# Optimization experiments

Hardware: AMD Instinct MI355X
Metric: run time of the kernel (lower is better)

## Reference

```python
import jax, jax.numpy as jnp
import numpy as np

EPS = 1e-5

def _dh_grid(b):
    # Driscoll-Healy beta grid + quadrature weights (includes sin(beta))
    k = np.arange(2 * b)
    beta = np.pi * (2 * k + 1) / (4 * b)
    j = np.arange(b)
    w = (2.0 / b) * np.sin(beta) * (np.sin(np.outer(beta, 2 * j + 1)) / (2 * j + 1)).sum(1)
    return beta, w

def _wigner_stack(L, betas):
    # d^l_{m m'}(beta) for l<L, zero-padded to slots j=m+(L-1) in a [L,nb,2L-1,2L-1] array.
    betas = np.atleast_1d(np.asarray(betas, np.float64))
    nb = betas.shape[0]
    J = 2 * L - 1
    out = np.zeros((L, nb, J, J), np.float64)
    for l in range(L):
        if l == 0:
            d = np.ones((nb, 1, 1))
        else:
            m = np.arange(-l, l + 1)
            c = np.sqrt(l * (l + 1) - m[:-1] * (m[:-1] + 1.0))
            Jp = np.diag(c, -1).astype(complex)  # raising operator in m=-l..l basis
            Jy = (Jp - Jp.T) / 2j
            ev, V = np.linalg.eigh(Jy)
            ph = np.exp(-1j * betas[:, None] * ev[None, :])
            d = np.einsum('mk,bk,nk->bmn', V, ph, V.conj()).real
        s = (L - 1) - l
        out[l, :, s:s + 2 * l + 1, s:s + 2 * l + 1] = d
    return out

def _constants():
    C = {}
    # layer1: S2 conv b 64 -> 20
    beta1, wq1 = _dh_grid(64)
    d1 = _wigner_stack(20, beta1)
    C['s2_ana'] = jnp.asarray((d1[:, :, :, 19] * wq1[None, :, None] * (2 * np.pi / 128)).astype(np.float32))  # [20,128,39]
    C['half1'] = jnp.asarray(_wigner_stack(20, np.pi / 2)[:, 0, :, 19].astype(np.float32))  # [20,39]
    beta_o1, wq2 = _dh_grid(20)
    ls1 = (2 * np.arange(20) + 1.0)
    C['syn1'] = jnp.asarray((_wigner_stack(20, beta_o1) * ls1[:, None, None, None]).astype(np.float32))  # [20,40,39,39]
    # layer2: SO3 conv b 20 -> 10
    d2 = _wigner_stack(10, beta_o1)
    C['ana2'] = jnp.asarray((d2 * wq2[None, :, None, None] * (2 * np.pi / 40) ** 2).astype(np.float32))  # [10,40,19,19]
    C['half2'] = jnp.asarray(_wigner_stack(10, np.pi / 2)[:, 0].astype(np.float32))  # [10,19,19]
    beta_o2, wq3 = _dh_grid(10)
    ls2 = (2 * np.arange(10) + 1.0)
    C['syn2'] = jnp.asarray((_wigner_stack(10, beta_o2) * ls2[:, None, None, None]).astype(np.float32))  # [10,20,19,19]
    # layer3: SO3 conv b 10 -> 7
    C['ana3'] = jnp.asarray((_wigner_stack(7, beta_o2) * wq3[None, :, None, None] * (2 * np.pi / 20) ** 2).astype(np.float32))  # [7,20,13,13]
    C['half3'] = jnp.asarray(_wigner_stack(7, np.pi / 2)[:, 0].astype(np.float32))  # [7,13,13]
    beta_o3, _ = _dh_grid(7)
    ls3 = (2 * np.arange(7) + 1.0)
    C['syn3'] = jnp.asarray((_wigner_stack(7, beta_o3) * ls3[:, None, None, None]).astype(np.float32))  # [7,14,13,13]
    return C

_C = _constants()

def _so3_ifft(Z, L, d_syn):
    # Z: [L, J, J, B, O] spectral (zero padded); output [B, O, 2L(beta), 2L(alpha), 2L(gamma)]
    M = jnp.einsum('lkjn,ljnbo->bokjn', d_syn, Z)
    N = 2 * L
    J = 2 * L - 1
    idx = (np.arange(J) - (L - 1)) % N
    S = jnp.zeros(M.shape[:3] + (N, N), M.dtype).at[..., idx[:, None], idx[None, :]].set(M)
    return jnp.fft.fft2(S, axes=(-2, -1)).real

def _s2_conv(x, w, bias, C):
    # x: [B, F, 2b_in(beta), 2b_in(alpha)] -> [B, O, 2*20, 2*20, 2*20]
    B, F, K, N = x.shape
    L = 20
    J = 2 * L - 1
    m = np.arange(J) - (L - 1)
    xh = jnp.fft.fft(x, axis=-1)[..., m % N]                       # [B,F,K,J]
    Fx = jnp.einsum('lkj,bfkj->ljbf', C['s2_ana'], xh)             # spherical FFT
    P = w.shape[-1]
    alpha = 2 * np.pi * np.arange(P) / P
    e = jnp.asarray(np.exp(-1j * np.outer(m, alpha)).astype(np.complex64))
    scale = 1.0 / np.sqrt(P * F)
    Ky = jnp.einsum('lj,jp,fop->ljfo', C['half1'], e, w * scale)   # kernel RFT on equatorial grid
    Z = jnp.einsum('ljbf,lnfo->ljnbo', Fx, jnp.conj(Ky))           # s2_mm (outer product over m,n)
    return _so3_ifft(Z, L, C['syn1']) + bias[None, :, None, None, None]

def _so3_conv(x, w, bias, Lo, ana, half, syn):
    # x: [B, F, K(beta), N(alpha), N(gamma)] -> [B, O, 2Lo, 2Lo, 2Lo]
    B, F, K, N, _ = x.shape
    J = 2 * Lo - 1
    m = np.arange(J) - (Lo - 1)
    idx = (-m) % N
    xh = jnp.fft.fft2(x, axes=(-2, -1))[..., idx[:, None], idx[None, :]]  # [B,F,K,J,J]
    Fx = jnp.einsum('lkjn,bfkjn->ljnbf', ana, xh)                  # SO3 FFT
    P = w.shape[-1]
    alpha = 2 * np.pi * np.arange(P) / P
    e = jnp.asarray(np.exp(1j * np.outer(m, alpha)).astype(np.complex64))
    scale = 1.0 / np.sqrt(P * F)
    Ky = jnp.einsum('ljn,jp,fop->ljnfo', half, e, w * scale)       # kernel RFT (beta=pi/2, gamma=0 grid)
    Z = jnp.einsum('ljkbf,lnkfo->ljnbo', Fx, jnp.conj(Ky))         # so3_mm: Z_{mn}=sum_k Fx_{mk} conj(Ky_{nk})
    return _so3_ifft(Z, Lo, syn) + bias[None, :, None, None, None]

def _bn(x, gamma, beta):
    axes = (0,) + tuple(range(2, x.ndim))
    mu = x.mean(axes, keepdims=True)
    var = x.var(axes, keepdims=True)
    shp = (1, -1) + (1,) * (x.ndim - 2)
    return (x - mu) * jax.lax.rsqrt(var + EPS) * gamma.reshape(shp) + beta.reshape(shp)

def _forward(x, w1, b1, g1, bt1, w2, b2, g2, bt2, w3, b3, g3, bt3, w_out, b_out):
    x = _s2_conv(x, w1, b1, _C)
    x = jax.nn.relu(_bn(x, g1, bt1))
    x = _so3_conv(x, w2, b2, 10, _C['ana2'], _C['half2'], _C['syn2'])
    x = jax.nn.relu(_bn(x, g2, bt2))
    x = _so3_conv(x, w3, b3, 7, _C['ana3'], _C['half3'], _C['syn3'])
    x = jax.nn.relu(_bn(x, g3, bt3))
    x = x.reshape(x.shape[0], x.shape[1], -1).max(-1)              # global max pool over SO3 grid
    mu = x.mean(0, keepdims=True)
    var = x.var(0, keepdims=True)
    x = (x - mu) * jax.lax.rsqrt(var + EPS)                        # BatchNorm1d(affine=False)
    x = x @ w_out + b_out
    return jax.nn.log_softmax(x, axis=1)

def setup_inputs():
    key = jax.random.key(0)
    ks = jax.random.split(key, 6)
    B = 16
    return {
        'x': jax.random.normal(ks[0], (B, 6, 128, 128), jnp.float32),
        'w1': jax.random.normal(ks[1], (6, 20, 128), jnp.float32),
        'b1': jnp.zeros((20,), jnp.float32),
        'g1': jnp.ones((20,), jnp.float32),
        'bt1': jnp.zeros((20,), jnp.float32),
        'w2': jax.random.normal(ks[2], (20, 60, 40), jnp.float32),
        'b2': jnp.zeros((60,), jnp.float32),
        'g2': jnp.ones((60,), jnp.float32),
        'bt2': jnp.zeros((60,), jnp.float32),
        'w3': jax.random.normal(ks[3], (60, 100, 20), jnp.float32),
        'b3': jnp.zeros((100,), jnp.float32),
        'g3': jnp.ones((100,), jnp.float32),
        'bt3': jnp.zeros((100,), jnp.float32),
        'w_out': jax.random.normal(ks[4], (100, 55), jnp.float32) * 0.1,
        'b_out': jnp.zeros((55,), jnp.float32),
    }

def reference(x, w1, b1, g1, bt1, w2, b2, g2, bt2, w3, b3, g3, bt3, w_out, b_out):
    return _forward(x, w1, b1, g1, bt1, w2, b2, g2, bt2, w3, b3, g3, bt3, w_out, b_out)
```

## Files before the change

kernel.cpp:

```cpp
#include <hip/hip_runtime.h>
#include <math.h>

#define PI 3.14159265358979323846

__device__ inline int iabs(int x){ return x < 0 ? -x : x; }

__device__ inline void cadd_mul(float2& acc, float2 a, float2 b){
    acc.x += a.x*b.x - a.y*b.y;
    acc.y += a.x*b.y + a.y*b.x;
}
__device__ inline void cadd_mulc(float2& acc, float2 a, float2 b){
    acc.x += a.x*b.x + a.y*b.y;
    acc.y += a.y*b.x - a.x*b.y;
}

__device__ inline double dpowi(double x, int n){
    double r = 1.0;
    for (int i = 0; i < n; ++i) r *= x;
    return r;
}

__device__ double wigner_d(int l, int a, int b, double beta, const double* sf)
{
    double cb = cos(0.5*beta), sb = sin(0.5*beta);
    int smin = max(0, b - a);
    int smax = min(l + b, l - a);
    if (smin > smax) return 0.0;
    double pref = sqrt(sf[l+a]*sf[l-a]*sf[l+b]*sf[l-b]);
    double t = dpowi(cb, 2*l + b - a - 2*smin) * dpowi(sb, a - b + 2*smin);
    if ((a - b + smin) & 1) t = -t;
    double r = -(sb*sb)/(cb*cb);
    double sum = 0.0;
    for (int s = smin; s <= smax; ++s){
        sum += t / (sf[l+b-s]*sf[s]*sf[a-b+s]*sf[l-a-s]);
        t *= r;
    }
    return pref * sum;
}

__global__ void k_wq(double* wq)
{
    int i = blockIdx.x*blockDim.x + threadIdx.x;
    int b, k, off;
    if (i < 128){ b = 64; k = i;      off = 0;   }
    else if (i < 168){ b = 20; k = i-128; off = 128; }
    else if (i < 188){ b = 10; k = i-168; off = 168; }
    else return;
    double beta = PI*(2*k+1)/(4.0*b);
    double s = 0.0;
    for (int j = 0; j < b; ++j) s += sin((2*j+1)*beta)/(2*j+1);
    wq[off+k] = (2.0/b)*sin(beta)*s;
}

__global__ void k_wig_full(float* __restrict__ out, const double* __restrict__ wq,
                           int L, int J, int NB, double denom, double beta_fix,
                           double factor, int mul2l1, int klayout)
{
    __shared__ double sf[40];
    if (threadIdx.x == 0){ sf[0]=1.0; for (int i=1;i<40;i++) sf[i]=sf[i-1]*i; }
    __syncthreads();
    int idx = blockIdx.x*blockDim.x + threadIdx.x;
    int total = L*NB*J*J;
    if (idx >= total) return;
    int n = idx % J;
    int j = (idx/J) % J;
    int k = (idx/(J*J)) % NB;
    int l = idx/(J*J*NB);
    int c0 = (J-1)/2;
    int mj = j - c0, mn = n - c0;
    float v = 0.f;
    if (iabs(mj) <= l && iabs(mn) <= l){
        double beta = (denom > 0.0) ? PI*(2*k+1)/denom : beta_fix;
        double d = wigner_d(l, mj, mn, beta, sf);
        double mlt = factor * (mul2l1 ? (2.0*l + 1.0) : 1.0);
        if (wq) mlt *= wq[k];
        v = (float)(d*mlt);
    }
    size_t oidx = klayout ? ((size_t)(k*L + l)*J + j)*J + n
                          : ((size_t)(l*NB + k)*J + j)*J + n;
    out[oidx] = v;
}

__global__ void k_wig_col(float* __restrict__ out, const double* __restrict__ wq,
                          int L, int J, int NB, double denom, double beta_fix, double factor)
{
    __shared__ double sf[40];
    if (threadIdx.x == 0){ sf[0]=1.0; for (int i=1;i<40;i++) sf[i]=sf[i-1]*i; }
    __syncthreads();
    int idx = blockIdx.x*blockDim.x + threadIdx.x;
    int total = L*NB*J;
    if (idx >= total) return;
    int j = idx % J;
    int k = (idx/J) % NB;
    int l = idx/(J*NB);
    int mj = j - (J-1)/2;
    float v = 0.f;
    if (iabs(mj) <= l){
        double beta = (denom > 0.0) ? PI*(2*k+1)/denom : beta_fix;
        double d = wigner_d(l, mj, 0, beta, sf);
        double mlt = factor;
        if (wq) mlt *= wq[k];
        v = (float)(d*mlt);
    }
    out[idx] = v;
}

__global__ void k_expmat(float2* __restrict__ out, int R, int C, int r0, int c0, int N, double sgn)
{
    int i = blockIdx.x*blockDim.x + threadIdx.x;
    if (i >= R*C) return;
    int c = i % C, r = i / C;
    double ang = sgn*2.0*PI * (double)((r - r0)*(c - c0)) / (double)N;
    out[i] = make_float2((float)cos(ang), (float)sin(ang));
}

__global__ __launch_bounds__(256) void k_dft1(const float* __restrict__ x,
    const float2* __restrict__ E1, float2* __restrict__ xh)
{
    __shared__ float2 sE[4992];
    __shared__ float rows[2048];
    int r0 = blockIdx.x * 16;
    int tid = threadIdx.x;
    for (int i = tid; i < 4992; i += 256) sE[i] = E1[i];
    for (int i = tid; i < 2048; i += 256) rows[i] = x[(size_t)r0*128 + i];
    __syncthreads();
    for (int i = tid; i < 320; i += 256){
        int jj = i % 20, kl = i / 20;
        int j = jj + 19;
        const float* row = &rows[kl*128];
        float2 acc = make_float2(0.f, 0.f);
        for (int a = 0; a < 128; ++a){
            float v = row[a];
            float2 e = sE[a*39 + j];
            acc.x += v*e.x; acc.y += v*e.y;
        }
        xh[(size_t)(r0 + kl)*39 + j] = acc;
    }
}

__global__ void k_fx1(const float* __restrict__ ana, const float2* __restrict__ xh,
                      float2* __restrict__ Fx)
{
    int i = blockIdx.x*blockDim.x + threadIdx.x;
    if (i >= 400) return;
    int hj = i % 20, l = i / 20;
    int j = hj + 19;
    int bf = blockIdx.y;
    const float*  ar = ana + (size_t)l*4992 + j;
    const float2* xr = xh + (size_t)bf*4992 + j;
    float2 acc = make_float2(0.f, 0.f);
    for (int k = 0; k < 128; ++k){
        float a = ar[k*39];
        float2 v = xr[k*39];
        acc.x += a*v.x; acc.y += a*v.y;
    }
    Fx[(size_t)(l*39 + j)*96 + bf] = acc;
}

__global__ void k_wh(float2* __restrict__ wh, const float* __restrict__ w,
                     int J, int P, int F, int O, double sgn)
{
    __shared__ float2 tw[128];
    int tid = threadIdx.x;
    if (tid < P){
        double a = sgn*2.0*PI*tid/P;
        tw[tid] = make_float2((float)cos(a), (float)sin(a));
    }
    __syncthreads();
    int idx = blockIdx.x*blockDim.x + tid;
    if (idx >= J*F*O) return;
    int o = idx % O;
    int f = (idx/O) % F;
    int j = idx/(O*F);
    int mj = j - (J-1)/2;
    int step = ((mj % P) + P) % P;
    const float* wr = w + (f*O+o)*P;
    float2 acc = make_float2(0.f, 0.f);
    int t = 0;
    for (int p = 0; p < P; ++p){
        float v = wr[p];
        acc.x += v*tw[t].x; acc.y += v*tw[t].y;
        t += step; if (t >= P) t -= P;
    }
    wh[idx] = acc;
}

__global__ void k_z1(const float2* __restrict__ Fx, const float2* __restrict__ wh,
                     const float* __restrict__ half1, float2* __restrict__ Z1c, int b0)
{
    int i = blockIdx.x*blockDim.x + threadIdx.x;
    if (i >= 15600) return;
    int bo = blockIdx.y;
    int n = i % 39;
    int lh = i / 39;
    int hj = lh % 20, l = lh / 20;
    int j = hj + 19;
    int b = b0 + bo/20, o = bo % 20;
    float h = half1[l*39 + n] * (1.f/sqrtf(128.f*6.f));
    const float2* fx = Fx + (size_t)(l*39 + j)*96 + b*6;
    const float2* wv = wh + (size_t)n*120 + o;
    float2 acc = make_float2(0.f, 0.f);
    for (int f = 0; f < 6; ++f) cadd_mulc(acc, fx[f], wv[(size_t)f*20]);
    Z1c[(size_t)bo*15600 + i] = make_float2(acc.x*h, acc.y*h);
}

template<int L, int J, int K, int N, int O, int BS>
__global__ __launch_bounds__(BS) void k_idft_t(const float2* __restrict__ Z,
    const float* __restrict__ syn, const float2* __restrict__ W,
    const float* __restrict__ bias, float* __restrict__ out)
{
    constexpr int JJ = J*J, NN = N*N, c0 = (J-1)/2;
    constexpr int JH = (J+1)/2;
    constexpr int LHJ = L*JH*J;
    __shared__ float2 sM[JH*J];
    __shared__ float2 sT[JH*N];
    __shared__ float2 sW[J*N];
    int bid = blockIdx.x;
    int k = bid % K;
    int bo = bid / K;
    int tid = threadIdx.x;

    for (int i = tid; i < J*N; i += BS) sW[i] = W[i];

    for (int i = tid; i < JH*J; i += BS){
        int n = i % J, hj = i / J;
        int lmin = max(hj, iabs(n-c0));
        float2 acc = make_float2(0.f, 0.f);
        const float2* zrow = Z + (size_t)bo*LHJ + i;
        const float*  srow = syn + (size_t)k*L*JJ + (size_t)c0*J + i;
        for (int l = lmin; l < L; ++l){
            float s = srow[(size_t)l*JJ];
            float2 z = zrow[(size_t)l*(JH*J)];
            acc.x += s*z.x; acc.y += s*z.y;
        }
        sM[i] = acc;
    }
    __syncthreads();

    constexpr int RT = (JH+1)/2, CT = N/2;
    for (int t = tid; t < RT*CT; t += BS){
        int tg = t % CT, tj = t / CT;
        int h0 = tj*2, g0 = tg*2;
        int h1 = (h0+1 < JH) ? h0+1 : h0;
        float2 a00 = make_float2(0.f,0.f), a01 = make_float2(0.f,0.f);
        float2 a10 = make_float2(0.f,0.f), a11 = make_float2(0.f,0.f);
        for (int n = 0; n < J; ++n){
            float2 w0 = sW[n*N+g0], w1 = sW[n*N+g0+1];
            float2 m0 = sM[h0*J+n], m1 = sM[h1*J+n];
            cadd_mul(a00, m0, w0); cadd_mul(a01, m0, w1);
            cadd_mul(a10, m1, w0); cadd_mul(a11, m1, w1);
        }
        sT[h0*N+g0] = a00; sT[h0*N+g0+1] = a01;
        if (h0+1 < JH){ sT[(h0+1)*N+g0] = a10; sT[(h0+1)*N+g0+1] = a11; }
    }
    __syncthreads();

    float bb = bias[bo % O];
    float* obase = out + (size_t)bid*NN;
    for (int t = tid; t < CT*CT; t += BS){
        int tg = t % CT, ta = t / CT;
        int a0 = ta*2, g0 = tg*2;
        float2 t00 = sT[g0], t01 = sT[g0+1];
        float r00 = t00.x, r01 = t01.x, r10 = t00.x, r11 = t01.x;
        for (int hj = 1; hj < JH; ++hj){
            float2 wa0 = sW[(c0+hj)*N+a0], wa1 = sW[(c0+hj)*N+a0+1];
            float2 t0 = sT[hj*N+g0], t1 = sT[hj*N+g0+1];
            r00 += 2.f*(t0.x*wa0.x - t0.y*wa0.y);
            r01 += 2.f*(t1.x*wa0.x - t1.y*wa0.y);
            r10 += 2.f*(t0.x*wa1.x - t0.y*wa1.y);
            r11 += 2.f*(t1.x*wa1.x - t1.y*wa1.y);
        }
        obase[(a0+0)*N+g0]   = r00 + bb;
        obase[(a0+0)*N+g0+1] = r01 + bb;
        obase[(a0+1)*N+g0]   = r10 + bb;
        obase[(a0+1)*N+g0+1] = r11 + bb;
    }
}

__global__ __launch_bounds__(256) void k_bn_stats(const float4* __restrict__ x, double* __restrict__ part,
                                                  int B, int C, int S4, int parts)
{
    int c = blockIdx.y, p = blockIdx.x;
    int chunk = (S4 + parts - 1)/parts;
    int s0 = p*chunk, s1e = min(S4, s0 + chunk);
    double a1 = 0.0, a2 = 0.0;
    for (int b = 0; b < B; ++b){
        const float4* base = x + ((size_t)b*C + c)*S4;
        for (int s = s0 + threadIdx.x; s < s1e; s += 256){
            float4 v = base[s];
            a1 += (double)v.x + (double)v.y + (double)v.z + (double)v.w;
            a2 += (double)v.x*v.x + (double)v.y*v.y + (double)v.z*v.z + (double)v.w*v.w;
        }
    }
    __shared__ double r1[256], r2[256];
    r1[threadIdx.x] = a1; r2[threadIdx.x] = a2;
    __syncthreads();
    for (int off = 128; off > 0; off >>= 1){
        if (threadIdx.x < off){ r1[threadIdx.x] += r1[threadIdx.x+off]; r2[threadIdx.x] += r2[threadIdx.x+off]; }
        __syncthreads();
    }
    if (threadIdx.x == 0){ int bid = p*C + c; part[2*bid] = r1[0]; part[2*bid+1] = r2[0]; }
}

__global__ void k_bn_fin(const double* __restrict__ part, const float* __restrict__ g,
                         const float* __restrict__ bt, float2* __restrict__ scsh,
                         int C, int parts, double cnt)
{
    int c = blockIdx.x*blockDim.x + threadIdx.x;
    if (c >= C) return;
    double s1 = 0.0, s2 = 0.0;
    for (int p = 0; p < parts; ++p){ s1 += part[2*(p*C+c)]; s2 += part[2*(p*C+c)+1]; }
    double mu = s1/cnt;
    double var = s2/cnt - mu*mu;
    float sc = (float)(1.0/sqrt(var + 1e-5)) * g[c];
    float sh = bt[c] - (float)mu*sc;
    scsh[c] = make_float2(sc, sh);
}

__global__ __launch_bounds__(256) void k_bn_apply(float4* __restrict__ x, const float2* __restrict__ scsh,
                                                  int C, int S4)
{
    int bc = blockIdx.y;
    float2 p = scsh[bc % C];
    size_t base = (size_t)bc * S4;
    for (int s = blockIdx.x*256 + threadIdx.x; s < S4; s += gridDim.x*256){
        float4 v = x[base + s];
        v.x = fmaxf(fmaf(v.x, p.x, p.y), 0.f);
        v.y = fmaxf(fmaf(v.y, p.x, p.y), 0.f);
        v.z = fmaxf(fmaf(v.z, p.x, p.y), 0.f);
        v.w = fmaxf(fmaf(v.w, p.x, p.y), 0.f);
        x[base + s] = v;
    }
}

template<int N, int J>
__global__ __launch_bounds__(256) void k_dft2_t(const float* __restrict__ x, float2* __restrict__ xh,
                                                const float2* __restrict__ EF)
{
    constexpr int JH = (J+1)/2, c0 = (J-1)/2;
    constexpr int NP = N+1;
    __shared__ float tile[N*NP];
    __shared__ float2 sT[N*J];
    __shared__ float2 sE[N*J];
    int bid = blockIdx.x;
    int tid = threadIdx.x;
    const float* src = x + (size_t)bid*N*N;
    for (int i = tid; i < N*N; i += 256){
        int a = i / N, g = i % N;
        tile[a*NP + g] = src[i];
    }
    for (int i = tid; i < N*J; i += 256) sE[i] = EF[i];
    __syncthreads();
    constexpr int AT = N/2, NT = (J+1)/2;
    for (int t = tid; t < AT*NT; t += 256){
        int tn = t % NT, ta = t / NT;
        int a0 = 2*ta, n0 = 2*tn;
        int n1 = (n0+1 < J) ? n0+1 : n0;
        float2 a00 = make_float2(0.f,0.f), a01 = make_float2(0.f,0.f);
        float2 a10 = make_float2(0.f,0.f), a11 = make_float2(0.f,0.f);
        const float* r0 = &tile[a0*NP];
        const float* r1 = &tile[(a0+1)*NP];
        for (int g = 0; g < N; ++g){
            float v0 = r0[g], v1 = r1[g];
            float2 e0 = sE[g*J+n0], e1 = sE[g*J+n1];
            a00.x += v0*e0.x; a00.y += v0*e0.y;
            a01.x += v0*e1.x; a01.y += v0*e1.y;
            a10.x += v1*e0.x; a10.y += v1*e0.y;
            a11.x += v1*e1.x; a11.y += v1*e1.y;
        }
        sT[a0*J+n0] = a00; sT[(a0+1)*J+n0] = a10;
        if (n0+1 < J){ sT[a0*J+n0+1] = a01; sT[(a0+1)*J+n0+1] = a11; }
    }
    __syncthreads();
    for (int t = tid; t < JH*NT; t += 256){
        int tn = t % NT, hj = t / NT;
        int n0 = 2*tn;
        int n1 = (n0+1 < J) ? n0+1 : n0;
        int j = c0 + hj;
        float2 a0 = make_float2(0.f,0.f), a1 = make_float2(0.f,0.f);
        for (int a = 0; a < N; ++a){
            float2 t0 = sT[a*J+n0], t1 = sT[a*J+n1];
            float2 e = sE[a*J+j];
            cadd_mul(a0, t0, e); cadd_mul(a1, t1, e);
        }
        float2* dst = xh + (size_t)bid*J*J + (size_t)j*J;
        dst[n0] = a0;
        if (n0+1 < J) dst[n0+1] = a1;
    }
}

__global__ void k_fx(const float* __restrict__ ana, const float2* __restrict__ xh,
                     float2* __restrict__ Fx, int L, int J, int JH, int K, int BF)
{
    int i = blockIdx.x*blockDim.x + threadIdx.x;
    int JJ = J*J;
    int total = L*JH*J;
    if (i >= total) return;
    int bf = blockIdx.y;
    int n = i % J;
    int hj = (i / J) % JH;
    int l = i / (J*JH);
    int c0 = (J-1)/2;
    int jn = (c0+hj)*J + n;
    const float*  ar = ana + (size_t)l*K*JJ + jn;
    const float2* xr = xh + (size_t)bf*K*JJ + jn;
    float2 acc = make_float2(0.f, 0.f);
    for (int k = 0; k < K; ++k){
        float a = ar[(size_t)k*JJ];
        float2 v = xr[(size_t)k*JJ];
        acc.x += a*v.x; acc.y += a*v.y;
    }
    Fx[((size_t)l*JJ + jn)*BF + bf] = acc;
}

__global__ void k_h(const float* __restrict__ half, const float2* __restrict__ Fx,
                    float2* __restrict__ H, int L, int J, int JH, int BF)
{
    int idx = blockIdx.x*blockDim.x + threadIdx.x;
    int total = L*JH*J*BF;
    if (idx >= total) return;
    int bf = idx % BF;
    int n = (idx/BF) % J;
    int hj = (idx/(BF*J)) % JH;
    int l = idx/(BF*J*JH);
    int c0 = (J-1)/2;
    int j = c0 + hj;
    const float* hr = half + (l*J+n)*J;
    const float2* fr = Fx + (size_t)(l*J+j)*J*BF + bf;
    float2 acc = make_float2(0.f, 0.f);
    for (int k = 0; k < J; ++k){
        float h = hr[k];
        float2 v = fr[(size_t)k*BF];
        acc.x += h*v.x; acc.y += h*v.y;
    }
    H[((size_t)(l*J+j)*J + n)*BF + bf] = acc;
}

__global__ __launch_bounds__(256) void k_zg(const float2* __restrict__ H,
    const float2* __restrict__ wh, float2* __restrict__ Z,
    int L, int J, int JH, int B, int F, int O, float scale)
{
    extern __shared__ float2 smem[];
    float2* swh = smem;
    float2* sH  = smem + F*O;
    int n = blockIdx.x;
    int b = blockIdx.y;
    int tid = threadIdx.x;
    int c0 = (J-1)/2;
    int LH = L*JH;
    int FO = F*O;
    const float2* whn = wh + (size_t)n*FO;
    for (int i = tid; i < FO; i += 256) swh[i] = whn[i];
    for (int i = tid; i < LH*F; i += 256){
        int f = i % F, lh = i / F;
        int l = lh / JH, hj = lh % JH;
        int lj = l*J + c0 + hj;
        sH[f*LH + lh] = H[((size_t)(lj*J + n)*B + b)*F + f];
    }
    __syncthreads();
    int total = O*LH;
    for (int i = tid; i < total; i += 256){
        int lh = i % LH, o = i / LH;
        float2 acc = make_float2(0.f, 0.f);
        for (int f = 0; f < F; ++f)
            cadd_mulc(acc, sH[f*LH + lh], swh[f*O + o]);
        Z[(size_t)(b*O + o)*LH*J + (size_t)lh*J + n] = make_float2(acc.x*scale, acc.y*scale);
    }
}

__global__ void k_pool(const float* __restrict__ x, float* __restrict__ pooled, int S)
{
    int bid = blockIdx.x;
    const float* base = x + (long long)bid*S;
    float m = -1e30f;
    for (int i = threadIdx.x; i < S; i += blockDim.x) m = fmaxf(m, base[i]);
    __shared__ float r[256];
    r[threadIdx.x] = m;
    __syncthreads();
    for (int off = 128; off > 0; off >>= 1){
        if (threadIdx.x < off) r[threadIdx.x] = fmaxf(r[threadIdx.x], r[threadIdx.x+off]);
        __syncthreads();
    }
    if (threadIdx.x == 0) pooled[bid] = r[0];
}

__global__ __launch_bounds__(256) void k_final(const float* __restrict__ pooled,
    const float* __restrict__ w, const float* __restrict__ bias, float* __restrict__ out)
{
    __shared__ float pn[1600];
    __shared__ float z[880];
    int tid = threadIdx.x;
    for (int f = tid; f < 100; f += 256){
        float s1 = 0.f, s2 = 0.f;
        for (int b = 0; b < 16; ++b){ float v = pooled[b*100+f]; s1 += v; s2 += v*v; }
        float mu = s1/16.f;
        float var = s2/16.f - mu*mu;
        float inv = rsqrtf(var + 1e-5f);
        for (int b = 0; b < 16; ++b) pn[b*100+f] = (pooled[b*100+f]-mu)*inv;
    }
    __syncthreads();
    for (int i = tid; i < 880; i += 256){
        int c = i % 55, b = i/55;
        float acc = bias[c];
        for (int f = 0; f < 100; ++f) acc += pn[b*100+f]*w[f*55+c];
        z[i] = acc;
    }
    __syncthreads();
    for (int b = tid; b < 16; b += 256){
        float m = -1e30f;
        for (int c = 0; c < 55; ++c) m = fmaxf(m, z[b*55+c]);
        float s = 0.f;
        for (int c = 0; c < 55; ++c) s += expf(z[b*55+c]-m);
        float lse = m + logf(s);
        for (int c = 0; c < 55; ++c) out[b*55+c] = z[b*55+c]-lse;
    }
}

static inline int cdiv(long long a, long long b){ return (int)((a + b - 1)/b); }

extern "C" void kernel_launch(void* const* d_in, const int* in_sizes, int n_in,
                              void* d_out, int out_size, void* d_ws, size_t ws_size,
                              hipStream_t stream)
{
    (void)in_sizes; (void)n_in; (void)out_size; (void)ws_size;
    const float* x   = (const float*)d_in[0];
    const float* w1  = (const float*)d_in[1];
    const float* b1  = (const float*)d_in[2];
    const float* g1  = (const float*)d_in[3];
    const float* bt1 = (const float*)d_in[4];
    const float* w2  = (const float*)d_in[5];
    const float* b2  = (const float*)d_in[6];
    const float* g2  = (const float*)d_in[7];
    const float* bt2 = (const float*)d_in[8];
    const float* w3  = (const float*)d_in[9];
    const float* b3  = (const float*)d_in[10];
    const float* g3  = (const float*)d_in[11];
    const float* bt3 = (const float*)d_in[12];
    const float* wo  = (const float*)d_in[13];
    const float* bo  = (const float*)d_in[14];
    float* out = (float*)d_out;
    float* ws  = (float*)d_ws;

    const size_t O_WQ    = 0;
    const size_t O_S2ANA = 376;
    const size_t O_HALF1 = 100216;
    const size_t O_SYN1  = 100996;
    const size_t O_ANA2  = 1317796;
    const size_t O_HALF2 = 1462196;
    const size_t O_SYN2  = 1465806;
    const size_t O_ANA3  = 1538006;
    const size_t O_HALF3 = 1561666;
    const size_t O_SYN3  = 1562849;
    const size_t O_STATS = 1579412;
    const size_t O_PART  = 1580132;
    const size_t O_EF2   = O_PART + 8192;
    const size_t O_EF3   = O_PART + 9712;
    const size_t O_POOL  = 1596516;
    const size_t O_XH1   = 1598116;
    const size_t O_FX1   = 2556580;
    const size_t O_WH1   = 2706340;
    const size_t O_WH2   = 2715700;
    const size_t O_WH3   = 2761300;
    const size_t O_W1    = 2917300;
    const size_t O_W2    = 2920420;
    const size_t O_W3    = 2921180;
    const size_t O_E1    = 2921544;
    const size_t O_A1    = 2931528;
    const size_t O_A2    = 23411528;

    double* WQd   = (double*)(ws + O_WQ);
    float*  S2ANA = ws + O_S2ANA;
    float*  HALF1 = ws + O_HALF1;
    float*  SYN1  = ws + O_SYN1;
    float*  ANA2  = ws + O_ANA2;
    float*  HALF2 = ws + O_HALF2;
    float*  SYN2  = ws + O_SYN2;
    float*  ANA3  = ws + O_ANA3;
    float*  HALF3 = ws + O_HALF3;
    float*  SYN3  = ws + O_SYN3;
    float2* SCSH  = (float2*)(ws + O_STATS);
    double* PART  = (double*)(ws + O_PART);
    float2* EF2   = (float2*)(ws + O_EF2);
    float2* EF3   = (float2*)(ws + O_EF3);
    float*  POOLED= ws + O_POOL;
    float2* XH1   = (float2*)(ws + O_XH1);
    float2* FX1   = (float2*)(ws + O_FX1);
    float2* WH1   = (float2*)(ws + O_WH1);
    float2* WH2   = (float2*)(ws + O_WH2);
    float2* WH3   = (float2*)(ws + O_WH3);
    float2* W1    = (float2*)(ws + O_W1);
    float2* W2    = (float2*)(ws + O_W2);
    float2* W3    = (float2*)(ws + O_W3);
    float2* E1    = (float2*)(ws + O_E1);
    float*  X1    = ws + O_A1;
    float2* FX2   = (float2*)(ws + O_A1);
    float2* H2    = (float2*)(ws + O_A1 + 2310400);
    float2* Z2    = (float2*)(ws + O_A1 + 4620800);
    float2* XH3   = (float2*)(ws + O_A1);
    float2* FX3   = (float2*)(ws + O_A1 + 6489600);
    float2* H3    = (float2*)(ws + O_A1 + 8760960);
    float2* Z3    = (float2*)(ws + O_A1 + 11032320);
    float2* Z1C   = (float2*)(ws + O_A2);
    float2* XH2   = (float2*)(ws + O_A2);
    float*  X2    = ws + O_A2;
    float*  X3    = ws + O_A2;

    const double F128 = 2.0*PI/128.0;
    const double F40sq = (2.0*PI/40.0)*(2.0*PI/40.0);
    const double F20sq = (2.0*PI/20.0)*(2.0*PI/20.0);

    k_wq<<<1, 256, 0, stream>>>(WQd);
    k_wig_col <<<cdiv(20*128*39,256),256,0,stream>>>(S2ANA, WQd,     20, 39, 128, 256.0, 0.0,   F128);
    k_wig_col <<<cdiv(20*39,256),    256,0,stream>>>(HALF1, nullptr, 20, 39, 1,   0.0,   PI/2,  1.0);
    k_wig_full<<<cdiv(1216800,256),  256,0,stream>>>(SYN1,  nullptr, 20, 39, 40,  80.0,  0.0,   1.0,   1, 1);
    k_wig_full<<<cdiv(144400,256),   256,0,stream>>>(ANA2,  WQd+128, 10, 19, 40,  80.0,  0.0,   F40sq, 0, 0);
    k_wig_full<<<cdiv(3610,256),     256,0,stream>>>(HALF2, nullptr, 10, 19, 1,   0.0,   PI/2,  1.0,   0, 0);
    k_wig_full<<<cdiv(72200,256),    256,0,stream>>>(SYN2,  nullptr, 10, 19, 20,  40.0,  0.0,   1.0,   1, 1);
    k_wig_full<<<cdiv(23660,256),    256,0,stream>>>(ANA3,  WQd+168, 7,  13, 20,  40.0,  0.0,   F20sq, 0, 0);
    k_wig_full<<<cdiv(1183,256),     256,0,stream>>>(HALF3, nullptr, 7,  13, 1,   0.0,   PI/2,  1.0,   0, 0);
    k_wig_full<<<cdiv(16562,256),    256,0,stream>>>(SYN3,  nullptr, 7,  13, 14,  28.0,  0.0,   1.0,   1, 1);
    k_expmat  <<<cdiv(1560,256),256,0,stream>>>(W1, 39, 40, 19, 0, 40, -1.0);
    k_expmat  <<<cdiv(380,256), 256,0,stream>>>(W2, 19, 20,  9, 0, 20, -1.0);
    k_expmat  <<<cdiv(182,256), 256,0,stream>>>(W3, 13, 14,  6, 0, 14, -1.0);
    k_expmat  <<<cdiv(4992,256),256,0,stream>>>(E1, 128, 39, 0, 19, 128, -1.0);
    k_expmat  <<<cdiv(760,256), 256,0,stream>>>(EF2, 40, 19, 0, 9, 40, +1.0);
    k_expmat  <<<cdiv(260,256), 256,0,stream>>>(EF3, 20, 13, 0, 6, 20, +1.0);

    k_dft1<<<768,256,0,stream>>>(x, E1, XH1);
    k_fx1 <<<dim3(2,96),256,0,stream>>>(S2ANA, XH1, FX1);
    k_wh  <<<cdiv(4680,256),  256,0,stream>>>(WH1, w1, 39, 128, 6, 20, -1.0);
    k_wh  <<<cdiv(22800,256), 256,0,stream>>>(WH2, w2, 19, 40, 20, 60, +1.0);
    k_wh  <<<cdiv(78000,256), 256,0,stream>>>(WH3, w3, 13, 20, 60, 100, +1.0);
    for (int c = 0; c < 2; ++c){
        int b0 = c*8;
        k_z1<<<dim3(cdiv(15600,256),160),256,0,stream>>>(FX1, WH1, HALF1, Z1C, b0);
        k_idft_t<20,39,40,40,20,256><<<160*40,256,0,stream>>>(Z1C, SYN1, W1, b1, X1 + (size_t)b0*20*64000);
    }
    k_bn_stats<<<dim3(32,20),256,0,stream>>>((const float4*)X1, PART, 16, 20, 16000, 32);
    k_bn_fin  <<<1,256,0,stream>>>(PART, g1, bt1, SCSH, 20, 32, 16.0*64000.0);
    k_bn_apply<<<dim3(cdiv(16000,256),320),256,0,stream>>>((float4*)X1, SCSH, 20, 16000);

    k_dft2_t<40,19><<<12800,256,0,stream>>>(X1, XH2, EF2);
    k_fx  <<<dim3(cdiv(1900,256),320),256,0,stream>>>(ANA2, XH2, FX2, 10, 19, 10, 40, 320);
    k_h   <<<cdiv(608000,256),256,0,stream>>>(HALF2, FX2, H2, 10, 19, 10, 320);
    k_zg  <<<dim3(19,16),256,(1200+2000)*sizeof(float2),stream>>>(H2, WH2, Z2, 10, 19, 10, 16, 20, 60, 1.f/sqrtf(800.f));
    k_idft_t<10,19,20,20,60,256><<<960*20,256,0,stream>>>(Z2, SYN2, W2, b2, X2);
    k_bn_stats<<<dim3(8,60),256,0,stream>>>((const float4*)X2, PART, 16, 60, 2000, 8);
    k_bn_fin  <<<1,256,0,stream>>>(PART, g2, bt2, SCSH+20, 60, 8, 16.0*8000.0);
    k_bn_apply<<<dim3(cdiv(2000,256),960),256,0,stream>>>((float4*)X2, SCSH+20, 60, 2000);

    k_dft2_t<20,13><<<19200,256,0,stream>>>(X2, XH3, EF3);
    k_fx  <<<dim3(cdiv(637,256),960),256,0,stream>>>(ANA3, XH3, FX3, 7, 13, 7, 20, 960);
    k_h   <<<cdiv(611520,256),256,0,stream>>>(HALF3, FX3, H3, 7, 13, 7, 960);
    k_zg  <<<dim3(13,16),256,(6000+2940)*sizeof(float2),stream>>>(H3, WH3, Z3, 7, 13, 7, 16, 60, 100, 1.f/sqrtf(1200.f));
    k_idft_t<7,13,14,14,100,256><<<1600*14,256,0,stream>>>(Z3, SYN3, W3, b3, X3);
    k_bn_stats<<<dim3(8,100),256,0,stream>>>((const float4*)X3, PART, 16, 100, 686, 8);
    k_bn_fin  <<<1,256,0,stream>>>(PART, g3, bt3, SCSH+80, 100, 8, 16.0*2744.0);
    k_bn_apply<<<dim3(cdiv(686,256),1600),256,0,stream>>>((float4*)X3, SCSH+80, 100, 686);

    k_pool <<<1600,256,0,stream>>>(X3, POOLED, 2744);
    k_final<<<1,256,0,stream>>>(POOLED, wo, bo, out);
}
```

Measured before the change: 1.053 ms.

## Batch multiple beta slices per block in inverse DFT and halve Wigner table generation

k_idft_t now handles KB beta indices per block. Each Z coefficient is loaded once and multiplied against several synthesis Wigner slices held in register accumulators, cutting redundant global reads of Z and the number of blocks. The Wigner table kernels gain a half-row mode that computes only the m>=0 rows, reducing setup work. Risks include higher register pressure, fewer blocks for occupancy, extra syncs per block, and unwritten lower-half table rows if any consumer reads them.

```diff
diff --git a/kernel.cpp b/kernel.cpp
--- a/kernel.cpp
+++ b/kernel.cpp
@@ -54,19 +54,21 @@
 
 __global__ void k_wig_full(float* __restrict__ out, const double* __restrict__ wq,
                            int L, int J, int NB, double denom, double beta_fix,
-                           double factor, int mul2l1, int klayout)
+                           double factor, int mul2l1, int klayout, int jhalf)
 {
     __shared__ double sf[40];
     if (threadIdx.x == 0){ sf[0]=1.0; for (int i=1;i<40;i++) sf[i]=sf[i-1]*i; }
     __syncthreads();
+    int c0 = (J-1)/2;
+    int JROWS = jhalf ? (J+1)/2 : J;
     int idx = blockIdx.x*blockDim.x + threadIdx.x;
-    int total = L*NB*J*J;
+    int total = L*NB*JROWS*J;
     if (idx >= total) return;
     int n = idx % J;
-    int j = (idx/J) % J;
-    int k = (idx/(J*J)) % NB;
-    int l = idx/(J*J*NB);
-    int c0 = (J-1)/2;
+    int jj = (idx/J) % JROWS;
+    int j = jhalf ? (c0 + jj) : jj;
+    int k = (idx/(J*JROWS)) % NB;
+    int l = idx/(J*JROWS*NB);
     int mj = j - c0, mn = n - c0;
     float v = 0.f;
     if (iabs(mj) <= l && iabs(mn) <= l){
@@ -82,18 +84,22 @@
 }
 
 __global__ void k_wig_col(float* __restrict__ out, const double* __restrict__ wq,
-                          int L, int J, int NB, double denom, double beta_fix, double factor)
+                          int L, int J, int NB, double denom, double beta_fix, double factor,
+                          int jhalf)
 {
     __shared__ double sf[40];
     if (threadIdx.x == 0){ sf[0]=1.0; for (int i=1;i<40;i++) sf[i]=sf[i-1]*i; }
     __syncthreads();
+    int c0 = (J-1)/2;
+    int JROWS = jhalf ? (J+1)/2 : J;
     int idx = blockIdx.x*blockDim.x + threadIdx.x;
-    int total = L*NB*J;
+    int total = L*NB*JROWS;
     if (idx >= total) return;
-    int j = idx % J;
-    int k = (idx/J) % NB;
-    int l = idx/(J*NB);
-    int mj = j - (J-1)/2;
+    int jj = idx % JROWS;
+    int j = jhalf ? (c0 + jj) : jj;
+    int k = (idx/JROWS) % NB;
+    int l = idx/(JROWS*NB);
+    int mj = j - c0;
     float v = 0.f;
     if (iabs(mj) <= l){
         double beta = (denom > 0.0) ? PI*(2*k+1)/denom : beta_fix;
@@ -102,7 +108,7 @@
         if (wq) mlt *= wq[k];
         v = (float)(d*mlt);
     }
-    out[idx] = v;
+    out[(size_t)(l*NB + k)*J + j] = v;
 }
 
 __global__ void k_expmat(float2* __restrict__ out, int R, int C, int r0, int c0, int N, double sgn)
@@ -204,76 +210,101 @@
     Z1c[(size_t)bo*15600 + i] = make_float2(acc.x*h, acc.y*h);
 }
 
-template<int L, int J, int K, int N, int O, int BS>
+template<int L, int J, int K, int KB, int N, int O, int BS>
 __global__ __launch_bounds__(BS) void k_idft_t(const float2* __restrict__ Z,
     const float* __restrict__ syn, const float2* __restrict__ W,
     const float* __restrict__ bias, float* __restrict__ out)
 {
     constexpr int JJ = J*J, NN = N*N, c0 = (J-1)/2;
     constexpr int JH = (J+1)/2;
-    constexpr int LHJ = L*JH*J;
-    __shared__ float2 sM[JH*J];
+    constexpr int JHJ = JH*J;
+    constexpr int LHJ = L*JHJ;
+    constexpr int KG = K/KB;
+    constexpr int SLOTS = (JHJ + BS - 1)/BS;
+    __shared__ float2 sM[KB*JHJ];
     __shared__ float2 sT[JH*N];
     __shared__ float2 sW[J*N];
     int bid = blockIdx.x;
-    int k = bid % K;
-    int bo = bid / K;
+    int kg = bid % KG;
+    int bo = bid / KG;
+    int k0 = kg*KB;
     int tid = threadIdx.x;
 
     for (int i = tid; i < J*N; i += BS) sW[i] = W[i];
 
-    for (int i = tid; i < JH*J; i += BS){
-        int n = i % J, hj = i / J;
-        int lmin = max(hj, iabs(n-c0));
-        float2 acc = make_float2(0.f, 0.f);
-        const float2* zrow = Z + (size_t)bo*LHJ + i;
-        const float*  srow = syn + (size_t)k*L*JJ + (size_t)c0*J + i;
-        for (int l = lmin; l < L; ++l){
-            float s = srow[(size_t)l*JJ];
-            float2 z = zrow[(size_t)l*(JH*J)];
-            acc.x += s*z.x; acc.y += s*z.y;
-        }
-        sM[i] = acc;
+    float2 acc[SLOTS][KB];
+    #pragma unroll
+    for (int s = 0; s < SLOTS; ++s)
+        #pragma unroll
+        for (int kb = 0; kb < KB; ++kb) acc[s][kb] = make_float2(0.f, 0.f);
+    #pragma unroll
+    for (int s = 0; s < SLOTS; ++s){
+        int i = tid + s*BS;
+        if (i < JHJ){
+            int n = i % J, hj = i / J;
+            int lmin = max(hj, iabs(n-c0));
+            const float2* zrow = Z + (size_t)bo*LHJ + i;
+            const float*  sbase = syn + (size_t)c0*J + i;
+            for (int l = lmin; l < L; ++l){
+                float2 z = zrow[(size_t)l*JHJ];
+                #pragma unroll
+                for (int kb = 0; kb < KB; ++kb){
+                    float s_ = sbase[(size_t)((k0+kb)*L + l)*JJ];
+                    acc[s][kb].x += s_*z.x; acc[s][kb].y += s_*z.y;
+                }
+            }
+        }
+    }
+    #pragma unroll
+    for (int s = 0; s < SLOTS; ++s){
+        int i = tid + s*BS;
+        if (i < JHJ){
+            #pragma unroll
+            for (int kb = 0; kb < KB; ++kb) sM[kb*JHJ + i] = acc[s][kb];
+        }
     }
     __syncthreads();
 
     constexpr int RT = (JH+1)/2, CT = N/2;
-    for (int t = tid; t < RT*CT; t += BS){
-        int tg = t % CT, tj = t / CT;
-        int h0 = tj*2, g0 = tg*2;
-        int h1 = (h0+1 < JH) ? h0+1 : h0;
-        float2 a00 = make_float2(0.f,0.f), a01 = make_float2(0.f,0.f);
-        float2 a10 = make_float2(0.f,0.f), a11 = make_float2(0.f,0.f);
-        for (int n = 0; n < J; ++n){
-            float2 w0 = sW[n*N+g0], w1 = sW[n*N+g0+1];
-            float2 m0 = sM[h0*J+n], m1 = sM[h1*J+n];
-            cadd_mul(a00, m0, w0); cadd_mul(a01, m0, w1);
-            cadd_mul(a10, m1, w0); cadd_mul(a11, m1, w1);
-        }
-        sT[h0*N+g0] = a00; sT[h0*N+g0+1] = a01;
-        if (h0+1 < JH){ sT[(h0+1)*N+g0] = a10; sT[(h0+1)*N+g0+1] = a11; }
-    }
-    __syncthreads();
-
-    float bb = bias[bo % O];
-    float* obase = out + (size_t)bid*NN;
-    for (int t = tid; t < CT*CT; t += BS){
-        int tg = t % CT, ta = t / CT;
-        int a0 = ta*2, g0 = tg*2;
-        float2 t00 = sT[g0], t01 = sT[g0+1];
-        float r00 = t00.x, r01 = t01.x, r10 = t00.x, r11 = t01.x;
-        for (int hj = 1; hj < JH; ++hj){
-            float2 wa0 = sW[(c0+hj)*N+a0], wa1 = sW[(c0+hj)*N+a0+1];
-            float2 t0 = sT[hj*N+g0], t1 = sT[hj*N+g0+1];
-            r00 += 2.f*(t0.x*wa0.x - t0.y*wa0.y);
-            r01 += 2.f*(t1.x*wa0.x - t1.y*wa0.y);
-            r10 += 2.f*(t0.x*wa1.x - t0.y*wa1.y);
-            r11 += 2.f*(t1.x*wa1.x - t1.y*wa1.y);
-        }
-        obase[(a0+0)*N+g0]   = r00 + bb;
-        obase[(a0+0)*N+g0+1] = r01 + bb;
-        obase[(a0+1)*N+g0]   = r10 + bb;
-        obase[(a0+1)*N+g0+1] = r11 + bb;
+    for (int kb = 0; kb < KB; ++kb){
+        const float2* sMk = &sM[kb*JHJ];
+        for (int t = tid; t < RT*CT; t += BS){
+            int tg = t % CT, tj = t / CT;
+            int h0 = tj*2, g0 = tg*2;
+            int h1 = (h0+1 < JH) ? h0+1 : h0;
+            float2 a00 = make_float2(0.f,0.f), a01 = make_float2(0.f,0.f);
+            float2 a10 = make_float2(0.f,0.f), a11 = make_float2(0.f,0.f);
+            for (int n = 0; n < J; ++n){
+                float2 w0 = sW[n*N+g0], w1 = sW[n*N+g0+1];
+                float2 m0 = sMk[h0*J+n], m1 = sMk[h1*J+n];
+                cadd_mul(a00, m0, w0); cadd_mul(a01, m0, w1);
+                cadd_mul(a10, m1, w0); cadd_mul(a11, m1, w1);
+            }
+            sT[h0*N+g0] = a00; sT[h0*N+g0+1] = a01;
+            if (h0+1 < JH){ sT[(h0+1)*N+g0] = a10; sT[(h0+1)*N+g0+1] = a11; }
+        }
+        __syncthreads();
+        float bb = bias[bo % O];
+        float* obase = out + ((size_t)bo*K + k0 + kb)*NN;
+        for (int t = tid; t < CT*CT; t += BS){
+            int tg = t % CT, ta = t / CT;
+            int a0 = ta*2, g0 = tg*2;
+            float2 t00 = sT[g0], t01 = sT[g0+1];
+            float r00 = t00.x, r01 = t01.x, r10 = t00.x, r11 = t01.x;
+            for (int hj = 1; hj < JH; ++hj){
+                float2 wa0 = sW[(c0+hj)*N+a0], wa1 = sW[(c0+hj)*N+a0+1];
+                float2 t0 = sT[hj*N+g0], t1 = sT[hj*N+g0+1];
+                r00 += 2.f*(t0.x*wa0.x - t0.y*wa0.y);
+                r01 += 2.f*(t1.x*wa0.x - t1.y*wa0.y);
+                r10 += 2.f*(t0.x*wa1.x - t0.y*wa1.y);
+                r11 += 2.f*(t1.x*wa1.x - t1.y*wa1.y);
+            }
+            obase[(a0+0)*N+g0]   = r00 + bb;
+            obase[(a0+0)*N+g0+1] = r01 + bb;
+            obase[(a0+1)*N+g0]   = r10 + bb;
+            obase[(a0+1)*N+g0+1] = r11 + bb;
+        }
+        __syncthreads();
     }
 }
 
@@ -610,15 +641,15 @@
     const double F20sq = (2.0*PI/20.0)*(2.0*PI/20.0);
 
     k_wq<<<1, 256, 0, stream>>>(WQd);
-    k_wig_col <<<cdiv(20*128*39,256),256,0,stream>>>(S2ANA, WQd,     20, 39, 128, 256.0, 0.0,   F128);
-    k_wig_col <<<cdiv(20*39,256),    256,0,stream>>>(HALF1, nullptr, 20, 39, 1,   0.0,   PI/2,  1.0);
-    k_wig_full<<<cdiv(1216800,256),  256,0,stream>>>(SYN1,  nullptr, 20, 39, 40,  80.0,  0.0,   1.0,   1, 1);
-    k_wig_full<<<cdiv(144400,256),   256,0,stream>>>(ANA2,  WQd+128, 10, 19, 40,  80.0,  0.0,   F40sq, 0, 0);
-    k_wig_full<<<cdiv(3610,256),     256,0,stream>>>(HALF2, nullptr, 10, 19, 1,   0.0,   PI/2,  1.0,   0, 0);
-    k_wig_full<<<cdiv(72200,256),    256,0,stream>>>(SYN2,  nullptr, 10, 19, 20,  40.0,  0.0,   1.0,   1, 1);
-    k_wig_full<<<cdiv(23660,256),    256,0,stream>>>(ANA3,  WQd+168, 7,  13, 20,  40.0,  0.0,   F20sq, 0, 0);
-    k_wig_full<<<cdiv(1183,256),     256,0,stream>>>(HALF3, nullptr, 7,  13, 1,   0.0,   PI/2,  1.0,   0, 0);
-    k_wig_full<<<cdiv(16562,256),    256,0,stream>>>(SYN3,  nullptr, 7,  13, 14,  28.0,  0.0,   1.0,   1, 1);
+    k_wig_col <<<cdiv(20*128*20,256),256,0,stream>>>(S2ANA, WQd,     20, 39, 128, 256.0, 0.0,   F128, 1);
+    k_wig_col <<<cdiv(20*39,256),    256,0,stream>>>(HALF1, nullptr, 20, 39, 1,   0.0,   PI/2,  1.0,  0);
+    k_wig_full<<<cdiv(624000,256),   256,0,stream>>>(SYN1,  nullptr, 20, 39, 40,  80.0,  0.0,   1.0,   1, 1, 1);
+    k_wig_full<<<cdiv(76000,256),    256,0,stream>>>(ANA2,  WQd+128, 10, 19, 40,  80.0,  0.0,   F40sq, 0, 0, 1);
+    k_wig_full<<<cdiv(3610,256),     256,0,stream>>>(HALF2, nullptr, 10, 19, 1,   0.0,   PI/2,  1.0,   0, 0, 0);
+    k_wig_full<<<cdiv(38000,256),    256,0,stream>>>(SYN2,  nullptr, 10, 19, 20,  40.0,  0.0,   1.0,   1, 1, 1);
+    k_wig_full<<<cdiv(12740,256),    256,0,stream>>>(ANA3,  WQd+168, 7,  13, 20,  40.0,  0.0,   F20sq, 0, 0, 1);
+    k_wig_full<<<cdiv(1183,256),     256,0,stream>>>(HALF3, nullptr, 7,  13, 1,   0.0,   PI/2,  1.0,   0, 0, 0);
+    k_wig_full<<<cdiv(8918,256),     256,0,stream>>>(SYN3,  nullptr, 7,  13, 14,  28.0,  0.0,   1.0,   1, 1, 1);
     k_expmat  <<<cdiv(1560,256),256,0,stream>>>(W1, 39, 40, 19, 0, 40, -1.0);
     k_expmat  <<<cdiv(380,256), 256,0,stream>>>(W2, 19, 20,  9, 0, 20, -1.0);
     k_expmat  <<<cdiv(182,256), 256,0,stream>>>(W3, 13, 14,  6, 0, 14, -1.0);
@@ -634,7 +665,7 @@
     for (int c = 0; c < 2; ++c){
         int b0 = c*8;
         k_z1<<<dim3(cdiv(15600,256),160),256,0,stream>>>(FX1, WH1, HALF1, Z1C, b0);
-        k_idft_t<20,39,40,40,20,256><<<160*40,256,0,stream>>>(Z1C, SYN1, W1, b1, X1 + (size_t)b0*20*64000);
+        k_idft_t<20,39,40,2,40,20,256><<<160*20,256,0,stream>>>(Z1C, SYN1, W1, b1, X1 + (size_t)b0*20*64000);
     }
     k_bn_stats<<<dim3(32,20),256,0,stream>>>((const float4*)X1, PART, 16, 20, 16000, 32);
     k_bn_fin  <<<1,256,0,stream>>>(PART, g1, bt1, SCSH, 20, 32, 16.0*64000.0);
@@ -644,7 +675,7 @@
     k_fx  <<<dim3(cdiv(1900,256),320),256,0,stream>>>(ANA2, XH2, FX2, 10, 19, 10, 40, 320);
     k_h   <<<cdiv(608000,256),256,0,stream>>>(HALF2, FX2, H2, 10, 19, 10, 320);
     k_zg  <<<dim3(19,16),256,(1200+2000)*sizeof(float2),stream>>>(H2, WH2, Z2, 10, 19, 10, 16, 20, 60, 1.f/sqrtf(800.f));
-    k_idft_t<10,19,20,20,60,256><<<960*20,256,0,stream>>>(Z2, SYN2, W2, b2, X2);
+    k_idft_t<10,19,20,5,20,60,256><<<960*4,256,0,stream>>>(Z2, SYN2, W2, b2, X2);
     k_bn_stats<<<dim3(8,60),256,0,stream>>>((const float4*)X2, PART, 16, 60, 2000, 8);
     k_bn_fin  <<<1,256,0,stream>>>(PART, g2, bt2, SCSH+20, 60, 8, 16.0*8000.0);
     k_bn_apply<<<dim3(cdiv(2000,256),960),256,0,stream>>>((float4*)X2, SCSH+20, 60, 2000);
@@ -653,7 +684,7 @@
     k_fx  <<<dim3(cdiv(637,256),960),256,0,stream>>>(ANA3, XH3, FX3, 7, 13, 7, 20, 960);
     k_h   <<<cdiv(611520,256),256,0,stream>>>(HALF3, FX3, H3, 7, 13, 7, 960);
     k_zg  <<<dim3(13,16),256,(6000+2940)*sizeof(float2),stream>>>(H3, WH3, Z3, 7, 13, 7, 16, 60, 100, 1.f/sqrtf(1200.f));
-    k_idft_t<7,13,14,14,100,256><<<1600*14,256,0,stream>>>(Z3, SYN3, W3, b3, X3);
+    k_idft_t<7,13,14,7,14,100,256><<<1600*2,256,0,stream>>>(Z3, SYN3, W3, b3, X3);
     k_bn_stats<<<dim3(8,100),256,0,stream>>>((const float4*)X3, PART, 16, 100, 686, 8);
     k_bn_fin  <<<1,256,0,stream>>>(PART, g3, bt3, SCSH+80, 100, 8, 16.0*2744.0);
     k_bn_apply<<<dim3(cdiv(686,256),1600),256,0,stream>>>((float4*)X3, SCSH+80, 100, 686);
```

After: 972.9 us. 7.6% less time.
